# Performance work log

Measured on AMD Instinct MI355X. Metric: run time of the kernel, lower is better.

The kernel has to match this reference:

```python
import jax, jax.numpy as jnp
import numpy as np


def setup_inputs() -> dict:
    key = jax.random.key(0)
    k1, k2, k3, k4 = jax.random.split(key, 4)
    B, T, C, H = 16, 2048, 384, 64
    x = jax.random.normal(k1, (B, T, C), dtype=jnp.float32)
    Wq = jax.random.normal(k2, (C, H), dtype=jnp.float32) * (1.0 / np.sqrt(C))
    Wk = jax.random.normal(k3, (C, H), dtype=jnp.float32) * (1.0 / np.sqrt(C))
    Wv = jax.random.normal(k4, (C, H), dtype=jnp.float32) * (1.0 / np.sqrt(C))
    return {"x": x, "Wq": Wq, "Wk": Wk, "Wv": Wv}


def reference(x, Wq, Wk, Wv):
    # x: [B, T, C]; Wq/Wk/Wv: [C, H]
    T = x.shape[1]
    H = Wk.shape[1]
    q = jnp.einsum('btc,ch->bth', x, Wq)
    k = jnp.einsum('btc,ch->bth', x, Wk)
    v = jnp.einsum('btc,ch->bth', x, Wv)
    scale = 1.0 / jnp.sqrt(jnp.asarray(H, dtype=x.dtype))
    wei = jnp.einsum('bth,bsh->bts', q, k) * scale  # [B, T, T]
    causal = jnp.tril(jnp.ones((T, T), dtype=bool))
    wei = jnp.where(causal, wei, -jnp.inf)
    attn = jax.nn.softmax(wei, axis=-1)
    # dropout p=0 -> identity
    out = jnp.einsum('bts,bsh->bth', attn, v)  # [B, T, H]
    return out
```

## Files before the change

### kernel.cpp

```cpp
#include <hip/hip_runtime.h>
#include <hip/hip_bf16.h>

#define B_ 16
#define T_ 2048
#define C_ 384
#define H_ 64

typedef __attribute__((ext_vector_type(8))) short short8;
typedef __attribute__((ext_vector_type(4))) short short4_t;
typedef __attribute__((ext_vector_type(4))) float floatx4;

static __device__ __forceinline__ short f2bf(float f) {
    unsigned u = __builtin_bit_cast(unsigned, f);
    u += 0x7FFF + ((u >> 16) & 1);
    return (short)(u >> 16);
}

__global__ void wt_kernel(const float* __restrict__ Wq, const float* __restrict__ Wk,
                          const float* __restrict__ Wv, short* __restrict__ wt) {
    int idx = blockIdx.x * 256 + threadIdx.x;
    if (idx >= 3 * H_ * C_) return;
    int mat = idx / (H_ * C_);
    int rem = idx - mat * (H_ * C_);
    int h = rem / C_;
    int c = rem - h * C_;
    const float* W = (mat == 0) ? Wq : ((mat == 1) ? Wk : Wv);
    wt[idx] = f2bf(W[c * H_ + h]);
}

__global__ __launch_bounds__(256) void qkv_kernel(
        const float* __restrict__ x, const short* __restrict__ wt,
        short* __restrict__ qo, short* __restrict__ ko, short* __restrict__ vto) {
    __shared__ short xs[64 * 392];

    int b = blockIdx.y, t0 = blockIdx.x * 64;
    int tid = threadIdx.x;

    const float* src = x + (size_t)(b * T_ + t0) * C_;
    for (int i = 0; i < 24; i++) {
        int chunk = i * 256 + tid;
        int row = chunk / 96, off = (chunk % 96) * 4;
        float4 f = *(const float4*)&src[row * 384 + off];
        short4_t s4;
        s4.x = f2bf(f.x); s4.y = f2bf(f.y); s4.z = f2bf(f.z); s4.w = f2bf(f.w);
        *(short4_t*)&xs[row * 392 + off] = s4;
    }
    __syncthreads();

    int w = tid >> 6, lane = tid & 63, quad = lane >> 4, l16 = lane & 15;

    floatx4 acc[4][3];
    for (int mt = 0; mt < 4; mt++)
        for (int j = 0; j < 3; j++) acc[mt][j] = (floatx4)0.0f;

    for (int kc = 0; kc < 384; kc += 32) {
        short8 a[4];
        for (int mt = 0; mt < 4; mt++)
            a[mt] = *(const short8*)&xs[(mt * 16 + l16) * 392 + kc + quad * 8];
        for (int j = 0; j < 3; j++) {
            int n = (w + 4 * j) * 16 + l16;
            short8 bf = *(const short8*)&wt[n * C_ + kc + quad * 8];
            for (int mt = 0; mt < 4; mt++)
                acc[mt][j] = __builtin_amdgcn_mfma_f32_16x16x32_bf16(a[mt], bf, acc[mt][j], 0, 0, 0);
        }
    }
    __syncthreads();

    {
        int h = w * 16 + l16;
        for (int j = 0; j < 3; j++)
            for (int mt = 0; mt < 4; mt++)
                for (int r = 0; r < 4; r++) {
                    int tl = mt * 16 + quad * 4 + r;
                    short bv = f2bf(acc[mt][j][r]);
                    if (j == 0)      xs[tl * 72 + h] = bv;
                    else if (j == 1) xs[4608 + tl * 72 + h] = bv;
                    else             xs[9216 + h * 72 + tl] = bv;
                }
    }
    __syncthreads();

    for (int i = 0; i < 6; i++) {
        int chunk = i * 256 + tid;
        int j = chunk >> 9, rem = chunk & 511;
        int row = rem >> 3, off = (rem & 7) * 8;
        short8 vdat = *(const short8*)&xs[j * 4608 + row * 72 + off];
        if (j == 0)      *(short8*)&qo[(size_t)(b * T_ + t0 + row) * H_ + off] = vdat;
        else if (j == 1) *(short8*)&ko[(size_t)(b * T_ + t0 + row) * H_ + off] = vdat;
        else             *(short8*)&vto[(size_t)(b * H_ + row) * T_ + t0 + off] = vdat;
    }
}

template<int SEG>
__global__ __launch_bounds__(256) void attn_seg_kernel(
        const short* __restrict__ q, const short* __restrict__ k,
        const short* __restrict__ vt, float* __restrict__ slots) {
    __shared__ short ks[64 * 72];
    __shared__ short vs[64 * 72];
    __shared__ short ps[4 * 16 * 72];

    int b = blockIdx.y, fid = blockIdx.x, nslot = gridDim.x;
    int tt = 0, cum = 0;
    while (cum + (tt / SEG + 1) <= fid) { cum += tt / SEG + 1; tt++; }
    int k0 = (fid - cum) * SEG;
    int k1 = min(k0 + SEG, tt + 1);

    int tid = threadIdx.x, w = tid >> 6, lane = tid & 63, quad = lane >> 4, l16 = lane & 15;
    int t0w = tt * 64 + w * 16;

    const short* qrow = q + (size_t)(b * T_ + t0w + l16) * H_;
    short8 aq0 = *(const short8*)&qrow[quad * 8];
    short8 aq1 = *(const short8*)&qrow[32 + quad * 8];

    floatx4 o[4];
    for (int nh = 0; nh < 4; nh++) o[nh] = (floatx4)0.0f;
    float lpart[4] = {0.f, 0.f, 0.f, 0.f};

    const short* kb0 = k + (size_t)b * T_ * H_;
    const short* vtb = vt + (size_t)b * H_ * T_;
    short* psw = ps + w * 16 * 72;

    int srow = tid >> 3, soff = (tid & 7) * 8;

    const float C1 = 0.125f * 1.44269504f;
    const float C2 = 12.0f * 1.44269504f;

    for (int st = k0; st < k1; st++) {
        int s0 = st * 64;
        const short* kg = kb0 + (size_t)s0 * H_;
        const short* vg = vtb + s0;
        *(short8*)&ks[srow * 72 + soff]        = *(const short8*)&kg[srow * H_ + soff];
        *(short8*)&ks[(srow + 32) * 72 + soff] = *(const short8*)&kg[(srow + 32) * H_ + soff];
        *(short8*)&vs[srow * 72 + soff]        = *(const short8*)&vg[(size_t)srow * T_ + soff];
        *(short8*)&vs[(srow + 32) * 72 + soff] = *(const short8*)&vg[(size_t)(srow + 32) * T_ + soff];
        __syncthreads();

        floatx4 sacc[4];
        for (int nt = 0; nt < 4; nt++) sacc[nt] = (floatx4)0.0f;
        for (int nt = 0; nt < 4; nt++) {
            short8 bk0 = *(const short8*)&ks[(nt * 16 + l16) * 72 + quad * 8];
            short8 bk1 = *(const short8*)&ks[(nt * 16 + l16) * 72 + 32 + quad * 8];
            sacc[nt] = __builtin_amdgcn_mfma_f32_16x16x32_bf16(aq0, bk0, sacc[nt], 0, 0, 0);
            sacc[nt] = __builtin_amdgcn_mfma_f32_16x16x32_bf16(aq1, bk1, sacc[nt], 0, 0, 0);
        }

        bool diag = (st == tt);
        for (int nt = 0; nt < 4; nt++) {
            int s_idx = s0 + nt * 16 + l16;
            for (int r = 0; r < 4; r++) {
                float p = exp2f(fmaf(sacc[nt][r], C1, -C2));
                if (diag && (s_idx > t0w + quad * 4 + r)) p = 0.0f;
                lpart[r] += p;
                psw[(quad * 4 + r) * 72 + nt * 16 + l16] = f2bf(p);
            }
        }

        short8 ap0 = *(const short8*)&psw[l16 * 72 + quad * 8];
        short8 ap1 = *(const short8*)&psw[l16 * 72 + 32 + quad * 8];
        for (int nh = 0; nh < 4; nh++) {
            short8 bv0 = *(const short8*)&vs[(nh * 16 + l16) * 72 + quad * 8];
            short8 bv1 = *(const short8*)&vs[(nh * 16 + l16) * 72 + 32 + quad * 8];
            o[nh] = __builtin_amdgcn_mfma_f32_16x16x32_bf16(ap0, bv0, o[nh], 0, 0, 0);
            o[nh] = __builtin_amdgcn_mfma_f32_16x16x32_bf16(ap1, bv1, o[nh], 0, 0, 0);
        }
        __syncthreads();
    }

    for (int d = 1; d < 16; d <<= 1)
        for (int r = 0; r < 4; r++)
            lpart[r] += __shfl_xor(lpart[r], d, 16);

    float* slot = slots + ((size_t)b * nslot + fid) * 4160;
    for (int nh = 0; nh < 4; nh++)
        for (int r = 0; r < 4; r++)
            slot[(w * 16 + quad * 4 + r) * 64 + nh * 16 + l16] = o[nh][r];
    if (l16 == 0)
        for (int r = 0; r < 4; r++)
            slot[4096 + w * 16 + quad * 4 + r] = lpart[r];
}

template<int SEG>
__global__ __launch_bounds__(256) void combine_kernel(
        const float* __restrict__ slots, int nslot, float* __restrict__ out) {
    int b = blockIdx.y, tt = blockIdx.x;
    int nseg = tt / SEG + 1;
    int cum = 0;
    for (int i = 0; i < tt; i++) cum += i / SEG + 1;
    const float* base = slots + ((size_t)b * nslot + cum) * 4160;

    int tid = threadIdx.x;
    int row = tid >> 2, c0 = (tid & 3) * 16;
    float4 acc[4] = {};
    float lsum = 0.f;
    for (int s = 0; s < nseg; s++) {
        const float* sp = base + (size_t)s * 4160;
        for (int i = 0; i < 4; i++) {
            float4 v = *(const float4*)&sp[row * 64 + c0 + i * 4];
            acc[i].x += v.x; acc[i].y += v.y; acc[i].z += v.z; acc[i].w += v.w;
        }
        lsum += sp[4096 + row];
    }
    float inv = 1.0f / lsum;
    float* op = out + (size_t)(b * T_ + tt * 64 + row) * H_ + c0;
    for (int i = 0; i < 4; i++) {
        float4 v;
        v.x = acc[i].x * inv; v.y = acc[i].y * inv;
        v.z = acc[i].z * inv; v.w = acc[i].w * inv;
        *(float4*)&op[i * 4] = v;
    }
}

template<bool DIAG>
static __device__ __forceinline__ void attn_step(
        int s0, int t0w, int quad, int l16,
        const short* __restrict__ kbase, const short* __restrict__ vtb,
        short8 aq0, short8 aq1, short* __restrict__ psw,
        floatx4 (&o)[4], float (&lpart)[4]) {
    floatx4 sacc[4];
    for (int nt = 0; nt < 4; nt++) sacc[nt] = (floatx4)0.0f;
    for (int nt = 0; nt < 4; nt++) {
        short8 bk0 = *(const short8*)&kbase[(nt * 16 + l16) * H_ + quad * 8];
        short8 bk1 = *(const short8*)&kbase[(nt * 16 + l16) * H_ + 32 + quad * 8];
        sacc[nt] = __builtin_amdgcn_mfma_f32_16x16x32_bf16(aq0, bk0, sacc[nt], 0, 0, 0);
        sacc[nt] = __builtin_amdgcn_mfma_f32_16x16x32_bf16(aq1, bk1, sacc[nt], 0, 0, 0);
    }
    const float C1 = 0.125f * 1.44269504f;
    const float C2 = 12.0f * 1.44269504f;
    for (int nt = 0; nt < 4; nt++) {
        int s_idx = s0 + nt * 16 + l16;
        for (int r = 0; r < 4; r++) {
            float p = exp2f(fmaf(sacc[nt][r], C1, -C2));
            if (DIAG && (s_idx > t0w + quad * 4 + r)) p = 0.0f;
            lpart[r] += p;
            psw[(quad * 4 + r) * 72 + nt * 16 + l16] = f2bf(p);
        }
    }
    short8 ap0 = *(const short8*)&psw[l16 * 72 + quad * 8];
    short8 ap1 = *(const short8*)&psw[l16 * 72 + 32 + quad * 8];
    for (int nh = 0; nh < 4; nh++) {
        short8 bv0 = *(const short8*)&vtb[(size_t)(nh * 16 + l16) * T_ + s0 + quad * 8];
        short8 bv1 = *(const short8*)&vtb[(size_t)(nh * 16 + l16) * T_ + s0 + 32 + quad * 8];
        o[nh] = __builtin_amdgcn_mfma_f32_16x16x32_bf16(ap0, bv0, o[nh], 0, 0, 0);
        o[nh] = __builtin_amdgcn_mfma_f32_16x16x32_bf16(ap1, bv1, o[nh], 0, 0, 0);
    }
}

__global__ __launch_bounds__(256) void attn_kernel(
        const short* __restrict__ q, const short* __restrict__ k,
        const short* __restrict__ vt, float* __restrict__ out) {
    __shared__ short ps[4 * 16 * 72];

    int b = blockIdx.y;
    int g = ((int)blockIdx.x + 4 * (b & 7)) & 31;
    int tt = (b < 8) ? g : 31 - g;
    int t0 = tt * 64;
    int tid = threadIdx.x, w = tid >> 6, lane = tid & 63, quad = lane >> 4, l16 = lane & 15;
    int t0w = t0 + w * 16;

    const short* qrow = q + (size_t)(b * T_ + t0w + l16) * H_;
    short8 aq0 = *(const short8*)&qrow[quad * 8];
    short8 aq1 = *(const short8*)&qrow[32 + quad * 8];

    floatx4 o[4];
    for (int nh = 0; nh < 4; nh++) o[nh] = (floatx4)0.0f;
    float lpart[4] = {0.f, 0.f, 0.f, 0.f};

    const short* kb0 = k + (size_t)b * T_ * H_;
    const short* vtb = vt + (size_t)b * H_ * T_;
    short* psw = ps + w * 16 * 72;

    for (int st = 0; st < tt; st++)
        attn_step<false>(st * 64, t0w, quad, l16, kb0 + (size_t)st * 64 * H_,
                         vtb, aq0, aq1, psw, o, lpart);
    attn_step<true>(tt * 64, t0w, quad, l16, kb0 + (size_t)tt * 64 * H_,
                    vtb, aq0, aq1, psw, o, lpart);

    for (int d = 1; d < 16; d <<= 1)
        for (int r = 0; r < 4; r++)
            lpart[r] += __shfl_xor(lpart[r], d, 16);

    for (int nh = 0; nh < 4; nh++)
        for (int r = 0; r < 4; r++) {
            int t = t0w + quad * 4 + r;
            out[(size_t)(b * T_ + t) * H_ + nh * 16 + l16] = o[nh][r] / lpart[r];
        }
}

extern "C" void kernel_launch(void* const* d_in, const int* in_sizes, int n_in,
                              void* d_out, int out_size, void* d_ws, size_t ws_size,
                              hipStream_t stream) {
    const float* x  = (const float*)d_in[0];
    const float* Wq = (const float*)d_in[1];
    const float* Wk = (const float*)d_in[2];
    const float* Wv = (const float*)d_in[3];

    char* ws = (char*)d_ws;
    short* qb  = (short*)(ws);
    short* kb  = (short*)(ws + (size_t)4 * 1024 * 1024);
    short* vtb = (short*)(ws + (size_t)8 * 1024 * 1024);
    short* wtb = (short*)(ws + (size_t)12 * 1024 * 1024);
    float* slots = (float*)(ws + (size_t)12 * 1024 * 1024 + 256 * 1024);
    size_t base_need = (size_t)12 * 1024 * 1024 + 256 * 1024;

    wt_kernel<<<dim3(288), dim3(256), 0, stream>>>(Wq, Wk, Wv, wtb);
    qkv_kernel<<<dim3(T_ / 64, B_), dim3(256), 0, stream>>>(x, wtb, qb, kb, vtb);

    float* out = (float*)d_out;
    auto fits = [&](int nslot) {
        return ws_size >= base_need + (size_t)B_ * nslot * 4160 * sizeof(float);
    };
    if (fits(144)) {
        attn_seg_kernel<4><<<dim3(144, B_), dim3(256), 0, stream>>>(qb, kb, vtb, slots);
        combine_kernel<4><<<dim3(T_ / 64, B_), dim3(256), 0, stream>>>(slots, 144, out);
    } else if (fits(80)) {
        attn_seg_kernel<8><<<dim3(80, B_), dim3(256), 0, stream>>>(qb, kb, vtb, slots);
        combine_kernel<8><<<dim3(T_ / 64, B_), dim3(256), 0, stream>>>(slots, 80, out);
    } else if (fits(48)) {
        attn_seg_kernel<16><<<dim3(48, B_), dim3(256), 0, stream>>>(qb, kb, vtb, slots);
        combine_kernel<16><<<dim3(T_ / 64, B_), dim3(256), 0, stream>>>(slots, 48, out);
    } else {
        attn_kernel<<<dim3(T_ / 64, B_), dim3(256), 0, stream>>>(qb, kb, vtb, out);
    }
}
```

Measured before the change: 141.6 us.

## Enlarge attention query tile to 128 rows and pre-swizzle QKV weights

The split-KV attention kernel now gives each block 128 query rows (32 per wave, two MFMA row tiles), so each K/V tile staged in shared memory is reused across twice as many queries. Segment bookkeeping, slot size and the combine kernel change to match, with a fixed 72 slots per batch. Separately, the weight-transpose kernel writes weights in a per-lane MFMA fragment order so the QKV projection loads them contiguously, and the projection now uses 32-row tiles with twice as many blocks. The cost is more registers per thread for the attention kernel and fewer attention blocks, which can lower occupancy and parallelism.

```diff
diff --git a/kernel.cpp b/kernel.cpp
--- a/kernel.cpp
+++ b/kernel.cpp
@@ -17,27 +17,30 @@
 }
 
 __global__ void wt_kernel(const float* __restrict__ Wq, const float* __restrict__ Wk,
-                          const float* __restrict__ Wv, short* __restrict__ wt) {
+                          const float* __restrict__ Wv, short* __restrict__ wt2) {
     int idx = blockIdx.x * 256 + threadIdx.x;
-    if (idx >= 3 * H_ * C_) return;
-    int mat = idx / (H_ * C_);
-    int rem = idx - mat * (H_ * C_);
-    int h = rem / C_;
-    int c = rem - h * C_;
+    if (idx >= 12 * 12 * 512) return;
+    int f = idx >> 9, within = idx & 511;
+    int lane = within >> 3, jj = within & 7;
+    int nt16 = f / 12, kc32 = f - nt16 * 12;
+    int mat = nt16 >> 2, w = nt16 & 3;
+    int quad = lane >> 4, l16 = lane & 15;
+    int h = w * 16 + l16;
+    int c = kc32 * 32 + quad * 8 + jj;
     const float* W = (mat == 0) ? Wq : ((mat == 1) ? Wk : Wv);
-    wt[idx] = f2bf(W[c * H_ + h]);
+    wt2[idx] = f2bf(W[c * H_ + h]);
 }
 
 __global__ __launch_bounds__(256) void qkv_kernel(
-        const float* __restrict__ x, const short* __restrict__ wt,
+        const float* __restrict__ x, const short* __restrict__ wt2,
         short* __restrict__ qo, short* __restrict__ ko, short* __restrict__ vto) {
-    __shared__ short xs[64 * 392];
-
-    int b = blockIdx.y, t0 = blockIdx.x * 64;
+    __shared__ short xs[32 * 392];
+
+    int b = blockIdx.y, t0 = blockIdx.x * 32;
     int tid = threadIdx.x;
 
     const float* src = x + (size_t)(b * T_ + t0) * C_;
-    for (int i = 0; i < 24; i++) {
+    for (int i = 0; i < 12; i++) {
         int chunk = i * 256 + tid;
         int row = chunk / 96, off = (chunk % 96) * 4;
         float4 f = *(const float4*)&src[row * 384 + off];
@@ -49,19 +52,18 @@
 
     int w = tid >> 6, lane = tid & 63, quad = lane >> 4, l16 = lane & 15;
 
-    floatx4 acc[4][3];
-    for (int mt = 0; mt < 4; mt++)
+    floatx4 acc[2][3];
+    for (int mt = 0; mt < 2; mt++)
         for (int j = 0; j < 3; j++) acc[mt][j] = (floatx4)0.0f;
 
     for (int kc = 0; kc < 384; kc += 32) {
-        short8 a[4];
-        for (int mt = 0; mt < 4; mt++)
-            a[mt] = *(const short8*)&xs[(mt * 16 + l16) * 392 + kc + quad * 8];
+        int kc32 = kc >> 5;
+        short8 a0 = *(const short8*)&xs[l16 * 392 + kc + quad * 8];
+        short8 a1 = *(const short8*)&xs[(16 + l16) * 392 + kc + quad * 8];
         for (int j = 0; j < 3; j++) {
-            int n = (w + 4 * j) * 16 + l16;
-            short8 bf = *(const short8*)&wt[n * C_ + kc + quad * 8];
-            for (int mt = 0; mt < 4; mt++)
-                acc[mt][j] = __builtin_amdgcn_mfma_f32_16x16x32_bf16(a[mt], bf, acc[mt][j], 0, 0, 0);
+            short8 bf = *(const short8*)&wt2[(((j * 4 + w) * 12) + kc32) * 512 + lane * 8];
+            acc[0][j] = __builtin_amdgcn_mfma_f32_16x16x32_bf16(a0, bf, acc[0][j], 0, 0, 0);
+            acc[1][j] = __builtin_amdgcn_mfma_f32_16x16x32_bf16(a1, bf, acc[1][j], 0, 0, 0);
         }
     }
     __syncthreads();
@@ -69,59 +71,62 @@
     {
         int h = w * 16 + l16;
         for (int j = 0; j < 3; j++)
-            for (int mt = 0; mt < 4; mt++)
+            for (int mt = 0; mt < 2; mt++)
                 for (int r = 0; r < 4; r++) {
                     int tl = mt * 16 + quad * 4 + r;
                     short bv = f2bf(acc[mt][j][r]);
                     if (j == 0)      xs[tl * 72 + h] = bv;
-                    else if (j == 1) xs[4608 + tl * 72 + h] = bv;
-                    else             xs[9216 + h * 72 + tl] = bv;
+                    else if (j == 1) xs[2304 + tl * 72 + h] = bv;
+                    else             xs[4608 + h * 40 + tl] = bv;
                 }
     }
     __syncthreads();
 
-    for (int i = 0; i < 6; i++) {
-        int chunk = i * 256 + tid;
-        int j = chunk >> 9, rem = chunk & 511;
-        int row = rem >> 3, off = (rem & 7) * 8;
-        short8 vdat = *(const short8*)&xs[j * 4608 + row * 72 + off];
-        if (j == 0)      *(short8*)&qo[(size_t)(b * T_ + t0 + row) * H_ + off] = vdat;
-        else if (j == 1) *(short8*)&ko[(size_t)(b * T_ + t0 + row) * H_ + off] = vdat;
-        else             *(short8*)&vto[(size_t)(b * H_ + row) * T_ + t0 + off] = vdat;
-    }
-}
-
-template<int SEG>
+    {
+        int row = tid >> 3, off = (tid & 7) * 8;
+        *(short8*)&qo[(size_t)(b * T_ + t0 + row) * H_ + off] = *(const short8*)&xs[row * 72 + off];
+        *(short8*)&ko[(size_t)(b * T_ + t0 + row) * H_ + off] = *(const short8*)&xs[2304 + row * 72 + off];
+    }
+    {
+        int h = tid >> 2, off = (tid & 3) * 8;
+        *(short8*)&vto[(size_t)(b * H_ + h) * T_ + t0 + off] = *(const short8*)&xs[4608 + h * 40 + off];
+    }
+}
+
 __global__ __launch_bounds__(256) void attn_seg_kernel(
         const short* __restrict__ q, const short* __restrict__ k,
         const short* __restrict__ vt, float* __restrict__ slots) {
     __shared__ short ks[64 * 72];
     __shared__ short vs[64 * 72];
-    __shared__ short ps[4 * 16 * 72];
+    __shared__ short ps[128 * 72];
 
     int b = blockIdx.y, fid = blockIdx.x, nslot = gridDim.x;
     int tt = 0, cum = 0;
-    while (cum + (tt / SEG + 1) <= fid) { cum += tt / SEG + 1; tt++; }
-    int k0 = (fid - cum) * SEG;
-    int k1 = min(k0 + SEG, tt + 1);
+    while (cum + ((2 * tt + 5) >> 2) <= fid) { cum += (2 * tt + 5) >> 2; tt++; }
+    int nk = 2 * tt + 2;
+    int k0 = (fid - cum) * 4;
+    int k1 = min(k0 + 4, nk);
 
     int tid = threadIdx.x, w = tid >> 6, lane = tid & 63, quad = lane >> 4, l16 = lane & 15;
-    int t0w = tt * 64 + w * 16;
-
-    const short* qrow = q + (size_t)(b * T_ + t0w + l16) * H_;
-    short8 aq0 = *(const short8*)&qrow[quad * 8];
-    short8 aq1 = *(const short8*)&qrow[32 + quad * 8];
-
-    floatx4 o[4];
-    for (int nh = 0; nh < 4; nh++) o[nh] = (floatx4)0.0f;
-    float lpart[4] = {0.f, 0.f, 0.f, 0.f};
+    int trow0 = tt * 128 + w * 32;
+
+    short8 aq[2][2];
+    for (int mt = 0; mt < 2; mt++) {
+        const short* qrow = q + (size_t)(b * T_ + trow0 + mt * 16 + l16) * H_;
+        aq[mt][0] = *(const short8*)&qrow[quad * 8];
+        aq[mt][1] = *(const short8*)&qrow[32 + quad * 8];
+    }
+
+    floatx4 o[2][4];
+    float lp[2][4];
+    for (int mt = 0; mt < 2; mt++)
+        for (int i = 0; i < 4; i++) { o[mt][i] = (floatx4)0.0f; lp[mt][i] = 0.f; }
 
     const short* kb0 = k + (size_t)b * T_ * H_;
     const short* vtb = vt + (size_t)b * H_ * T_;
-    short* psw = ps + w * 16 * 72;
+    short* psw = ps + w * 32 * 72;
 
     int srow = tid >> 3, soff = (tid & 7) * 8;
-
     const float C1 = 0.125f * 1.44269504f;
     const float C2 = 12.0f * 1.44269504f;
 
@@ -135,74 +140,85 @@
         *(short8*)&vs[(srow + 32) * 72 + soff] = *(const short8*)&vg[(size_t)(srow + 32) * T_ + soff];
         __syncthreads();
 
-        floatx4 sacc[4];
-        for (int nt = 0; nt < 4; nt++) sacc[nt] = (floatx4)0.0f;
+        floatx4 sacc[2][4];
+        for (int mt = 0; mt < 2; mt++)
+            for (int nt = 0; nt < 4; nt++) sacc[mt][nt] = (floatx4)0.0f;
         for (int nt = 0; nt < 4; nt++) {
             short8 bk0 = *(const short8*)&ks[(nt * 16 + l16) * 72 + quad * 8];
             short8 bk1 = *(const short8*)&ks[(nt * 16 + l16) * 72 + 32 + quad * 8];
-            sacc[nt] = __builtin_amdgcn_mfma_f32_16x16x32_bf16(aq0, bk0, sacc[nt], 0, 0, 0);
-            sacc[nt] = __builtin_amdgcn_mfma_f32_16x16x32_bf16(aq1, bk1, sacc[nt], 0, 0, 0);
-        }
-
-        bool diag = (st == tt);
-        for (int nt = 0; nt < 4; nt++) {
-            int s_idx = s0 + nt * 16 + l16;
-            for (int r = 0; r < 4; r++) {
-                float p = exp2f(fmaf(sacc[nt][r], C1, -C2));
-                if (diag && (s_idx > t0w + quad * 4 + r)) p = 0.0f;
-                lpart[r] += p;
-                psw[(quad * 4 + r) * 72 + nt * 16 + l16] = f2bf(p);
+            sacc[0][nt] = __builtin_amdgcn_mfma_f32_16x16x32_bf16(aq[0][0], bk0, sacc[0][nt], 0, 0, 0);
+            sacc[0][nt] = __builtin_amdgcn_mfma_f32_16x16x32_bf16(aq[0][1], bk1, sacc[0][nt], 0, 0, 0);
+            sacc[1][nt] = __builtin_amdgcn_mfma_f32_16x16x32_bf16(aq[1][0], bk0, sacc[1][nt], 0, 0, 0);
+            sacc[1][nt] = __builtin_amdgcn_mfma_f32_16x16x32_bf16(aq[1][1], bk1, sacc[1][nt], 0, 0, 0);
+        }
+
+        bool diag = (st >= 2 * tt);
+        for (int mt = 0; mt < 2; mt++)
+            for (int nt = 0; nt < 4; nt++) {
+                int s_idx = s0 + nt * 16 + l16;
+                for (int r = 0; r < 4; r++) {
+                    float p = exp2f(fmaf(sacc[mt][nt][r], C1, -C2));
+                    if (diag && (s_idx > trow0 + mt * 16 + quad * 4 + r)) p = 0.0f;
+                    lp[mt][r] += p;
+                    psw[(mt * 16 + quad * 4 + r) * 72 + nt * 16 + l16] = f2bf(p);
+                }
             }
-        }
-
-        short8 ap0 = *(const short8*)&psw[l16 * 72 + quad * 8];
-        short8 ap1 = *(const short8*)&psw[l16 * 72 + 32 + quad * 8];
+
+        short8 ap[2][2];
+        for (int mt = 0; mt < 2; mt++) {
+            ap[mt][0] = *(const short8*)&psw[(mt * 16 + l16) * 72 + quad * 8];
+            ap[mt][1] = *(const short8*)&psw[(mt * 16 + l16) * 72 + 32 + quad * 8];
+        }
         for (int nh = 0; nh < 4; nh++) {
             short8 bv0 = *(const short8*)&vs[(nh * 16 + l16) * 72 + quad * 8];
             short8 bv1 = *(const short8*)&vs[(nh * 16 + l16) * 72 + 32 + quad * 8];
-            o[nh] = __builtin_amdgcn_mfma_f32_16x16x32_bf16(ap0, bv0, o[nh], 0, 0, 0);
-            o[nh] = __builtin_amdgcn_mfma_f32_16x16x32_bf16(ap1, bv1, o[nh], 0, 0, 0);
+            o[0][nh] = __builtin_amdgcn_mfma_f32_16x16x32_bf16(ap[0][0], bv0, o[0][nh], 0, 0, 0);
+            o[0][nh] = __builtin_amdgcn_mfma_f32_16x16x32_bf16(ap[0][1], bv1, o[0][nh], 0, 0, 0);
+            o[1][nh] = __builtin_amdgcn_mfma_f32_16x16x32_bf16(ap[1][0], bv0, o[1][nh], 0, 0, 0);
+            o[1][nh] = __builtin_amdgcn_mfma_f32_16x16x32_bf16(ap[1][1], bv1, o[1][nh], 0, 0, 0);
         }
         __syncthreads();
     }
 
     for (int d = 1; d < 16; d <<= 1)
-        for (int r = 0; r < 4; r++)
-            lpart[r] += __shfl_xor(lpart[r], d, 16);
-
-    float* slot = slots + ((size_t)b * nslot + fid) * 4160;
-    for (int nh = 0; nh < 4; nh++)
-        for (int r = 0; r < 4; r++)
-            slot[(w * 16 + quad * 4 + r) * 64 + nh * 16 + l16] = o[nh][r];
+        for (int mt = 0; mt < 2; mt++)
+            for (int r = 0; r < 4; r++)
+                lp[mt][r] += __shfl_xor(lp[mt][r], d, 16);
+
+    float* slot = slots + ((size_t)b * nslot + fid) * 8320;
+    for (int mt = 0; mt < 2; mt++)
+        for (int nh = 0; nh < 4; nh++)
+            for (int r = 0; r < 4; r++)
+                slot[(w * 32 + mt * 16 + quad * 4 + r) * 64 + nh * 16 + l16] = o[mt][nh][r];
     if (l16 == 0)
-        for (int r = 0; r < 4; r++)
-            slot[4096 + w * 16 + quad * 4 + r] = lpart[r];
-}
-
-template<int SEG>
+        for (int mt = 0; mt < 2; mt++)
+            for (int r = 0; r < 4; r++)
+                slot[8192 + w * 32 + mt * 16 + quad * 4 + r] = lp[mt][r];
+}
+
 __global__ __launch_bounds__(256) void combine_kernel(
         const float* __restrict__ slots, int nslot, float* __restrict__ out) {
     int b = blockIdx.y, tt = blockIdx.x;
-    int nseg = tt / SEG + 1;
+    int nseg = (2 * tt + 5) >> 2;
     int cum = 0;
-    for (int i = 0; i < tt; i++) cum += i / SEG + 1;
-    const float* base = slots + ((size_t)b * nslot + cum) * 4160;
+    for (int i = 0; i < tt; i++) cum += (2 * i + 5) >> 2;
+    const float* base = slots + ((size_t)b * nslot + cum) * 8320;
 
     int tid = threadIdx.x;
-    int row = tid >> 2, c0 = (tid & 3) * 16;
-    float4 acc[4] = {};
+    int row = tid >> 1, c0 = (tid & 1) * 32;
+    float4 acc[8] = {};
     float lsum = 0.f;
     for (int s = 0; s < nseg; s++) {
-        const float* sp = base + (size_t)s * 4160;
-        for (int i = 0; i < 4; i++) {
+        const float* sp = base + (size_t)s * 8320;
+        for (int i = 0; i < 8; i++) {
             float4 v = *(const float4*)&sp[row * 64 + c0 + i * 4];
             acc[i].x += v.x; acc[i].y += v.y; acc[i].z += v.z; acc[i].w += v.w;
         }
-        lsum += sp[4096 + row];
+        lsum += sp[8192 + row];
     }
     float inv = 1.0f / lsum;
-    float* op = out + (size_t)(b * T_ + tt * 64 + row) * H_ + c0;
-    for (int i = 0; i < 4; i++) {
+    float* op = out + (size_t)(b * T_ + tt * 128 + row) * H_ + c0;
+    for (int i = 0; i < 8; i++) {
         float4 v;
         v.x = acc[i].x * inv; v.y = acc[i].y * inv;
         v.z = acc[i].z * inv; v.w = acc[i].w * inv;
@@ -303,21 +319,13 @@
     size_t base_need = (size_t)12 * 1024 * 1024 + 256 * 1024;
 
     wt_kernel<<<dim3(288), dim3(256), 0, stream>>>(Wq, Wk, Wv, wtb);
-    qkv_kernel<<<dim3(T_ / 64, B_), dim3(256), 0, stream>>>(x, wtb, qb, kb, vtb);
+    qkv_kernel<<<dim3(T_ / 32, B_), dim3(256), 0, stream>>>(x, wtb, qb, kb, vtb);
 
     float* out = (float*)d_out;
-    auto fits = [&](int nslot) {
-        return ws_size >= base_need + (size_t)B_ * nslot * 4160 * sizeof(float);
-    };
-    if (fits(144)) {
-        attn_seg_kernel<4><<<dim3(144, B_), dim3(256), 0, stream>>>(qb, kb, vtb, slots);
-        combine_kernel<4><<<dim3(T_ / 64, B_), dim3(256), 0, stream>>>(slots, 144, out);
-    } else if (fits(80)) {
-        attn_seg_kernel<8><<<dim3(80, B_), dim3(256), 0, stream>>>(qb, kb, vtb, slots);
-        combine_kernel<8><<<dim3(T_ / 64, B_), dim3(256), 0, stream>>>(slots, 80, out);
-    } else if (fits(48)) {
-        attn_seg_kernel<16><<<dim3(48, B_), dim3(256), 0, stream>>>(qb, kb, vtb, slots);
-        combine_kernel<16><<<dim3(T_ / 64, B_), dim3(256), 0, stream>>>(slots, 48, out);
+    const int NSLOT = 72;
+    if (ws_size >= base_need + (size_t)B_ * NSLOT * 8320 * sizeof(float)) {
+        attn_seg_kernel<<<dim3(NSLOT, B_), dim3(256), 0, stream>>>(qb, kb, vtb, slots);
+        combine_kernel<<<dim3(T_ / 128, B_), dim3(256), 0, stream>>>(slots, NSLOT, out);
     } else {
         attn_kernel<<<dim3(T_ / 64, B_), dim3(256), 0, stream>>>(qb, kb, vtb, out);
     }
```

Result: no change. 143.3 us (+1.2%).
